# Performance work log

Measured on AMD Instinct MI355X. Metric: run time of the kernel, lower is better.

The kernel has to match this reference:

```python
import jax, jax.numpy as jnp
import numpy as np
from jax import lax

THR = 1.0
BETA = 0.9
SLOPE = 25.0  # fast_sigmoid surrogate slope
N_JOINTS = 6

@jax.custom_vjp
def spike_fn(x):
    # Heaviside forward, fast_sigmoid surrogate backward (snntorch surrogate.fast_sigmoid)
    return (x > 0).astype(x.dtype)

def _spike_fwd(x):
    return spike_fn(x), x

def _spike_bwd(x, g):
    return (g / (SLOPE * jnp.abs(x) + 1.0) ** 2,)

spike_fn.defvjp(_spike_fwd, _spike_bwd)

def lif(cur, mem):
    # snntorch Leaky, reset_mechanism='subtract': reset from previous mem (detached)
    reset = lax.stop_gradient(spike_fn(mem - THR))
    mem = BETA * mem + cur - reset * THR
    spk = spike_fn(mem - THR)
    return spk, mem

def rate_encode(data, u):
    # data: (B, F), u: (T, B, F) uniform[0,1) -> binary spikes (T, B, F)
    dmin = jnp.min(data, axis=1, keepdims=True)
    dmax = jnp.max(data, axis=1, keepdims=True)
    rng = dmax - dmin
    rng = jnp.where(rng == 0, jnp.ones_like(rng), rng)
    norm = (data - dmin) / rng
    prob = jnp.clip(100.0 * norm * 0.001, 0.0, 1.0)  # max_rate=100, dt=0.001
    return (u < prob[None]).astype(jnp.float32)

def conv1x1(x, W, b):
    # x: (B, Cin, H, 1), W: (Cout, Cin, 1, 1)
    y = lax.conv_general_dilated(x, W, (1, 1), 'VALID',
                                 dimension_numbers=('NCHW', 'OIHW', 'NCHW'))
    return y + b[None, :, None, None]

def setup_inputs() -> dict:
    key = jax.random.key(0)
    ks = jax.random.split(key, 16)
    B, T, n = 8192, 200, N_JOINTS
    inp = {
        'x':  jax.random.normal(ks[0], (B, 3 * n), jnp.float32),
        'u1': jax.random.uniform(ks[1], (T, B, 2 * n), jnp.float32),
        'u2': jax.random.uniform(ks[2], (T, B, n), jnp.float32),
        'u3': jax.random.uniform(ks[3], (T, B, n), jnp.float32),
        'W1': jax.random.normal(ks[4], (256, 12), jnp.float32) * 0.2,
        'b1': jax.random.normal(ks[5], (256,), jnp.float32) * 0.05,
        'W2': jax.random.normal(ks[6], (256, 256), jnp.float32) * 0.06,
        'b2': jax.random.normal(ks[7], (256,), jnp.float32) * 0.05,
        'W3': jax.random.normal(ks[8], (6, 256), jnp.float32) * 0.06,
        'b3': jax.random.normal(ks[9], (6,), jnp.float32) * 0.05,
        'Wc1': jax.random.normal(ks[10], (32, 3, 1, 1), jnp.float32) * 0.5,
        'bc1': jax.random.normal(ks[11], (32,), jnp.float32) * 0.05,
        'Wc2': jax.random.normal(ks[12], (64, 32, 1, 1), jnp.float32) * 0.15,
        'bc2': jax.random.normal(ks[13], (64,), jnp.float32) * 0.05,
        'WA': jax.random.normal(ks[14], (1, 64), jnp.float32) * 0.12,
    }
    return inp

def reference(x, u1, u2, u3, W1, b1, W2, b2, W3, b3, Wc1, bc1, Wc2, bc2, WA):
    n = N_JOINTS
    B = x.shape[0]
    spk_in = rate_encode(x[:, :2 * n], u1)        # (T, B, 2n)
    spk_thdot = rate_encode(x[:, n:2 * n], u2)    # (T, B, n)
    spk_thdot2 = rate_encode(x[:, 2 * n:], u3)    # (T, B, n)

    mem1 = jnp.zeros((B, 256), jnp.float32)
    mem2 = jnp.zeros((B, 256), jnp.float32)
    mem3 = jnp.zeros((B, n), jnp.float32)
    mem4 = jnp.zeros((B, 32, n, 1), jnp.float32)
    conv_out0 = jnp.zeros((B, 64, n, 1), jnp.float32)

    def step(carry, inp):
        m1, m2, m3, m4, _ = carry
        s_in, s_td, s_td2 = inp
        spk1, m1 = lif(s_in @ W1.T + b1, m1)
        spk2, m2 = lif(spk1 @ W2.T + b2, m2)
        spk3, m3 = lif(spk2 @ W3.T + b3, m3)
        spk_conv = jnp.stack([s_td, spk3, s_td2], axis=1)[..., None]  # (B,3,n,1)
        cur4 = conv1x1(spk_conv, Wc1, bc1)  # maxpool1 with k=1 is identity
        spk4, m4 = lif(cur4, m4)
        conv_out = conv1x1(spk4, Wc2, bc2)  # maxpool2 with k=1 is identity
        return (m1, m2, m3, m4, conv_out), None

    (_, _, _, _, conv_out), _ = lax.scan(step, (mem1, mem2, mem3, mem4, conv_out0),
                                         (spk_in, spk_thdot, spk_thdot2))
    # c.T: out_a/b/c = fc_A(conv_out[:, :, i, 0]) for i in 0..2, no bias
    c_t = jnp.einsum('bcm,c->bm', conv_out[:, :, :3, 0], WA[0])  # (B, 3)
    return c_t
```

## Files before the change

### kernel.cpp

```cpp
#include <hip/hip_runtime.h>
#include <cstdint>
#include <cstddef>

typedef unsigned long long u64;

__global__ void prep_weights(const float* __restrict__ W2, const float* __restrict__ Wc2,
                             const float* __restrict__ bc2, const float* __restrict__ WA,
                             float* __restrict__ Wt2f, double* __restrict__ wEff,
                             double* __restrict__ bEff)
{
  int id = blockIdx.x * 256 + (int)threadIdx.x;
  if (id < 65536){ int i = id >> 8, j = id & 255; Wt2f[(i<<8)+j] = W2[j*256+i]; }
  else if (id < 65792){ Wt2f[id] = 0.0f; }
  if (id < 32){ double s = 0.0; for (int c=0;c<64;c++) s += (double)WA[c]*(double)Wc2[c*32+id]; wEff[id] = s; }
  if (id == 32){ double s = 0.0; for (int c=0;c<64;c++) s += (double)WA[c]*(double)bc2[c]; *bEff = s; }
}

__global__ void prep_probs(const float* __restrict__ x, double* __restrict__ probs, int B)
{
  int b = blockIdx.x, k = (int)threadIdx.x;
  if (b >= B || k >= 24) return;
  double* pb = probs + (size_t)b*24;
  if (k >= 18){ pb[k] = -1.0; return; }
  int fk, g0, gn;
  if (k < 12){ fk = k;          g0 = 0;  gn = 12; }
  else if (k < 15){ fk = 6+(k-12);  g0 = 6;  gn = 6; }
  else           { fk = 12+(k-15); g0 = 12; gn = 6; }
  const float* xb = x + (size_t)b*18;
  double mn = (double)xb[g0], mx = mn;
  for (int f = 1; f < gn; f++){ double v = (double)xb[g0+f]; mn = fmin(mn, v); mx = fmax(mx, v); }
  double rng = mx - mn; if (rng == 0.0) rng = 1.0;
  double norm = ((double)xb[fk] - mn) / rng;
  double p = (100.0 * norm) * 0.001;
  p = fmin(fmax(p, 0.0), 1.0);
  pb[k] = p;
}

__global__ void prep_enc(const float* __restrict__ u1, const float* __restrict__ u2,
                         const float* __restrict__ u3, const double* __restrict__ probs,
                         unsigned* __restrict__ encT, int B, int T)
{
  int b = blockIdx.x * blockDim.x + (int)threadIdx.x;
  int t = blockIdx.y;
  if (b >= B) return;
  if (t >= T){ encT[(size_t)b*(T+2) + t] = 0u; return; }
  const double* pb = probs + (size_t)b*24;
  size_t r = (size_t)t * B + b;
  const float* a1 = u1 + r*12;
  const float* a2 = u2 + r*6;
  const float* a3 = u3 + r*6;
  unsigned e = 0;
  #pragma unroll
  for (int k = 0; k < 12; k++) if ((double)a1[k] < pb[k])    e |= (1u << k);
  #pragma unroll
  for (int h = 0; h < 3; h++)  if ((double)a2[h] < pb[12+h]) e |= (1u << (12+h));
  #pragma unroll
  for (int h = 0; h < 3; h++)  if ((double)a3[h] < pb[15+h]) e |= (1u << (15+h));
  encT[(size_t)b*(T+2) + t] = e;
}

__global__ __launch_bounds__(256) void snn_main(
    const unsigned* __restrict__ encT,
    const float* __restrict__ b1, const float* __restrict__ b2, const float* __restrict__ b3,
    const float* __restrict__ W1, const float* __restrict__ W3,
    const float* __restrict__ Wc1, const float* __restrict__ bc1,
    const float* __restrict__ Wt2f,
    const double* __restrict__ wEff, const double* __restrict__ bEff,
    float* __restrict__ out, int B, int T)
{
  __shared__ __align__(16) float s_w1[12*256];
  __shared__ __align__(16) float s_w3[257*4];

  const int tid  = (int)threadIdx.x;
  const int lane = tid & 63;
  const int wid  = tid >> 6;
  const int b = blockIdx.x * 4 + wid;
  const int l4 = lane << 2;
  const int lcl = (lane < 3) ? lane : 3;

  for (int i = tid; i < 3072; i += 256){ int k = i >> 8, j = i & 255; s_w1[i] = W1[j*12+k]; }
  for (int i = tid; i < 1028; i += 256){
    int r = i >> 2, c = i & 3;
    s_w3[i] = (r < 256 && c < 3) ? W3[c*256 + r] : 0.0f;
  }
  __syncthreads();
  if (b >= B) return;

  const float4 b1f = *(const float4*)(b1 + l4);
  const float4 b2f = *(const float4*)(b2 + l4);
  const double b1d0=b1f.x, b1d1=b1f.y, b1d2=b1f.z, b1d3=b1f.w;
  const double b2d0=b2f.x, b2d1=b2f.y, b2d2=b2f.z, b2d3=b2f.w;
  const double b3d = (lane < 3) ? (double)b3[lane] : 0.0;
  double wc1b=0.0, wEd=0.0, pre0=0.0, pre1=0.0, pre2=0.0, pre3=0.0;
  if (lane < 32){
    double wa = (double)Wc1[lane*3+0];
    wc1b      = (double)Wc1[lane*3+1];
    double wc = (double)Wc1[lane*3+2];
    double bd = (double)bc1[lane];
    wEd  = wEff[lane];
    pre0 = bd;
    pre1 = bd + wa;
    pre2 = bd + wc;
    pre3 = bd + wa + wc;
  }

  double m10=0,m11=0,m12=0,m13=0;
  double m20=0,m21=0,m22=0,m23=0;
  double m3v=0;
  double m40=0,m41=0,m42=0;
  bool sp20=false,sp21=false,sp22=false,sp23=false;
  bool sp3v=false;
  bool sp40=false,sp41=false,sp42=false;

  const unsigned* encTb = encT + (size_t)b * (T + 2);

  unsigned e_cur = __builtin_amdgcn_readfirstlane(encTb[0]);
  unsigned e_nx  = __builtin_amdgcn_readfirstlane(encTb[1]);
  double ca0=b1d0, ca1=b1d1, ca2=b1d2, ca3=b1d3;
  {
    unsigned w = e_cur & 0xFFFu;
    while (w){
      int k = __builtin_ctz(w); w &= w-1;
      const float4 r = *(const float4*)&s_w1[(k<<8) + l4];
      ca0 += (double)r.x; ca1 += (double)r.y; ca2 += (double)r.z; ca3 += (double)r.w;
    }
  }

  for (int t = 0; t < T; t++){
    m10 = fma(0.9, m10, ca0);
    m11 = fma(0.9, m11, ca1);
    m12 = fma(0.9, m12, ca2);
    m13 = fma(0.9, m13, ca3);
    const bool sp10 = m10 > 1.0; u64 w0 = __ballot(sp10);
    const bool sp11 = m11 > 1.0; u64 w1 = __ballot(sp11);
    const bool sp12 = m12 > 1.0; u64 w2 = __ballot(sp12);
    const bool sp13 = m13 > 1.0; u64 w3m = __ballot(sp13);

    int i0 = w0  ? (((int)__builtin_ctzll(w0) <<2)|0) : 256;  w0  &= w0 -1;
    int i1 = w1  ? (((int)__builtin_ctzll(w1) <<2)|1) : 256;  w1  &= w1 -1;
    int i2 = w2  ? (((int)__builtin_ctzll(w2) <<2)|2) : 256;  w2  &= w2 -1;
    int i3 = w3m ? (((int)__builtin_ctzll(w3m)<<2)|3) : 256;  w3m &= w3m-1;
    const float4 g0 = *(const float4*)(Wt2f + ((size_t)i0<<8) + l4);
    const float4 g1 = *(const float4*)(Wt2f + ((size_t)i1<<8) + l4);
    const float4 g2 = *(const float4*)(Wt2f + ((size_t)i2<<8) + l4);
    const float4 g3 = *(const float4*)(Wt2f + ((size_t)i3<<8) + l4);

    const unsigned e_n2 = encTb[t+2];

    ca0 = (sp10 ? -1.0 : 0.0) + b1d0;
    ca1 = (sp11 ? -1.0 : 0.0) + b1d1;
    ca2 = (sp12 ? -1.0 : 0.0) + b1d2;
    ca3 = (sp13 ? -1.0 : 0.0) + b1d3;
    {
      unsigned w = e_nx & 0xFFFu;
      while (w){
        int k = __builtin_ctz(w); w &= w-1;
        const float4 r = *(const float4*)&s_w1[(k<<8) + l4];
        ca0 += (double)r.x; ca1 += (double)r.y; ca2 += (double)r.z; ca3 += (double)r.w;
      }
    }

    double c0 = (sp20 ? -1.0 : 0.0) + b2d0;
    double c1 = (sp21 ? -1.0 : 0.0) + b2d1;
    double c2 = (sp22 ? -1.0 : 0.0) + b2d2;
    double c3 = (sp23 ? -1.0 : 0.0) + b2d3;
    if (i0 != 256){ c0 += (double)g0.x; c1 += (double)g0.y; c2 += (double)g0.z; c3 += (double)g0.w; }
    if (i1 != 256){ c0 += (double)g1.x; c1 += (double)g1.y; c2 += (double)g1.z; c3 += (double)g1.w; }
    if (i2 != 256){ c0 += (double)g2.x; c1 += (double)g2.y; c2 += (double)g2.z; c3 += (double)g2.w; }
    if (i3 != 256){ c0 += (double)g3.x; c1 += (double)g3.y; c2 += (double)g3.z; c3 += (double)g3.w; }

    while (w0 | w1 | w2 | w3m){
      int j0 = w0  ? (((int)__builtin_ctzll(w0) <<2)|0) : 256;  w0  &= w0 -1;
      int j1 = w1  ? (((int)__builtin_ctzll(w1) <<2)|1) : 256;  w1  &= w1 -1;
      int j2 = w2  ? (((int)__builtin_ctzll(w2) <<2)|2) : 256;  w2  &= w2 -1;
      int j3 = w3m ? (((int)__builtin_ctzll(w3m)<<2)|3) : 256;  w3m &= w3m-1;
      const float4 h0 = *(const float4*)(Wt2f + ((size_t)j0<<8) + l4);
      const float4 h1 = *(const float4*)(Wt2f + ((size_t)j1<<8) + l4);
      const float4 h2 = *(const float4*)(Wt2f + ((size_t)j2<<8) + l4);
      const float4 h3 = *(const float4*)(Wt2f + ((size_t)j3<<8) + l4);
      if (j0 != 256){ c0 += (double)h0.x; c1 += (double)h0.y; c2 += (double)h0.z; c3 += (double)h0.w; }
      if (j1 != 256){ c0 += (double)h1.x; c1 += (double)h1.y; c2 += (double)h1.z; c3 += (double)h1.w; }
      if (j2 != 256){ c0 += (double)h2.x; c1 += (double)h2.y; c2 += (double)h2.z; c3 += (double)h2.w; }
      if (j3 != 256){ c0 += (double)h3.x; c1 += (double)h3.y; c2 += (double)h3.z; c3 += (double)h3.w; }
    }

    m20 = fma(0.9, m20, c0);
    m21 = fma(0.9, m21, c1);
    m22 = fma(0.9, m22, c2);
    m23 = fma(0.9, m23, c3);
    sp20 = m20 > 1.0; u64 v0 = __ballot(sp20);
    sp21 = m21 > 1.0; u64 v1 = __ballot(sp21);
    sp22 = m22 > 1.0; u64 v2 = __ballot(sp22);
    sp23 = m23 > 1.0; u64 v3 = __ballot(sp23);

    double cl3 = (sp3v ? -1.0 : 0.0) + b3d;
    while (v0 | v1 | v2 | v3){
      int j0 = v0 ? (((int)__builtin_ctzll(v0)<<2)|0) : 256;  v0 &= v0-1;
      int j1 = v1 ? (((int)__builtin_ctzll(v1)<<2)|1) : 256;  v1 &= v1-1;
      int j2 = v2 ? (((int)__builtin_ctzll(v2)<<2)|2) : 256;  v2 &= v2-1;
      int j3 = v3 ? (((int)__builtin_ctzll(v3)<<2)|3) : 256;  v3 &= v3-1;
      if (j0 != 256) cl3 += (double)s_w3[(j0<<2) + lcl];
      if (j1 != 256) cl3 += (double)s_w3[(j1<<2) + lcl];
      if (j2 != 256) cl3 += (double)s_w3[(j2<<2) + lcl];
      if (j3 != 256) cl3 += (double)s_w3[(j3<<2) + lcl];
    }
    m3v = fma(0.9, m3v, cl3);
    sp3v = m3v > 1.0;
    const unsigned s3 = (unsigned)(__ballot((lane < 3) && sp3v) & 7ull);

    const unsigned td  = (e_cur >> 12) & 7u;
    const unsigned td2 = (e_cur >> 15) & 7u;
    {
      double cur, t1, t2;
      t1 = (td2 & 1u) ? pre2 : pre0;  t2 = (td2 & 1u) ? pre3 : pre1;
      cur = (td & 1u) ? t2 : t1;
      if (s3 & 1u) cur += wc1b;
      cur += sp40 ? -1.0 : 0.0;
      m40 = fma(0.9, m40, cur); sp40 = m40 > 1.0;
      t1 = (td2 & 2u) ? pre2 : pre0;  t2 = (td2 & 2u) ? pre3 : pre1;
      cur = (td & 2u) ? t2 : t1;
      if (s3 & 2u) cur += wc1b;
      cur += sp41 ? -1.0 : 0.0;
      m41 = fma(0.9, m41, cur); sp41 = m41 > 1.0;
      t1 = (td2 & 4u) ? pre2 : pre0;  t2 = (td2 & 4u) ? pre3 : pre1;
      cur = (td & 4u) ? t2 : t1;
      if (s3 & 4u) cur += wc1b;
      cur += sp42 ? -1.0 : 0.0;
      m42 = fma(0.9, m42, cur); sp42 = m42 > 1.0;
    }

    e_cur = e_nx;
    e_nx  = __builtin_amdgcn_readfirstlane(e_n2);
  }

  double o0 = sp40 ? wEd : 0.0;
  double o1 = sp41 ? wEd : 0.0;
  double o2 = sp42 ? wEd : 0.0;
  for (int off = 32; off > 0; off >>= 1){
    o0 += __shfl_xor(o0, off, 64);
    o1 += __shfl_xor(o1, off, 64);
    o2 += __shfl_xor(o2, off, 64);
  }
  if (lane == 0){
    const double be = *bEff;
    out[b*3+0] = (float)(o0 + be);
    out[b*3+1] = (float)(o1 + be);
    out[b*3+2] = (float)(o2 + be);
  }
}

extern "C" void kernel_launch(void* const* d_in, const int* in_sizes, int n_in,
                              void* d_out, int out_size, void* d_ws, size_t ws_size,
                              hipStream_t stream)
{
  const float* x   = (const float*)d_in[0];
  const float* u1  = (const float*)d_in[1];
  const float* u2  = (const float*)d_in[2];
  const float* u3  = (const float*)d_in[3];
  const float* W1  = (const float*)d_in[4];
  const float* b1  = (const float*)d_in[5];
  const float* W2  = (const float*)d_in[6];
  const float* b2  = (const float*)d_in[7];
  const float* W3  = (const float*)d_in[8];
  const float* b3  = (const float*)d_in[9];
  const float* Wc1 = (const float*)d_in[10];
  const float* bc1 = (const float*)d_in[11];
  const float* Wc2 = (const float*)d_in[12];
  const float* bc2 = (const float*)d_in[13];
  const float* WA  = (const float*)d_in[14];
  float* out = (float*)d_out;

  const int B = in_sizes[0] / 18;
  const int T = in_sizes[1] / (B * 12);

  char* ws = (char*)d_ws;
  float*  Wt2f  = (float*)(ws + 0);
  double* wEff  = (double*)(ws + 263168);
  double* bEff  = (double*)(ws + 263424);
  double* probs = (double*)(ws + 263432);
  unsigned* encT= (unsigned*)(ws + 263432 + (size_t)B*24*8);

  hipLaunchKernelGGL(prep_weights, dim3(257), dim3(256), 0, stream,
                     W2, Wc2, bc2, WA, Wt2f, wEff, bEff);
  hipLaunchKernelGGL(prep_probs, dim3(B), dim3(64), 0, stream, x, probs, B);
  hipLaunchKernelGGL(prep_enc, dim3((B+255)/256, T+2), dim3(256), 0, stream,
                     u1, u2, u3, probs, encT, B, T);
  hipLaunchKernelGGL(snn_main, dim3((B+3)/4), dim3(256), 0, stream,
                     encT, b1, b2, b3, W1, W3, Wc1, bc1, Wt2f, wEff, bEff, out, B, T);
}
```

Before: 684.1 us.

## Replace layer-1 sparse W1 accumulation with precomputed 6-bit subset-sum table lookups

Precomputes a table of double-precision partial sums of W1 columns for every 6-bit spike pattern (two halves of the 12 input bits), then replaces the per-step data-dependent loop over input spikes in shared memory with two table-row gathers from global memory, prefetched one step ahead. This removes the variable-length LDS loop and its per-bit conversions from the serial time loop. In exchange it adds a small prep kernel, 256 KB of workspace, and global/L2 loads of doubles each step. The summation order changes, which can alter rounding slightly.

Result: slower. 710.3 us (+3.8%).

```diff
diff --git a/kernel.cpp b/kernel.cpp
--- a/kernel.cpp
+++ b/kernel.cpp
@@ -14,6 +14,18 @@
   else if (id < 65792){ Wt2f[id] = 0.0f; }
   if (id < 32){ double s = 0.0; for (int c=0;c<64;c++) s += (double)WA[c]*(double)Wc2[c*32+id]; wEff[id] = s; }
   if (id == 32){ double s = 0.0; for (int c=0;c<64;c++) s += (double)WA[c]*(double)bc2[c]; *bEff = s; }
+}
+
+__global__ void prep_tab(const float* __restrict__ W1, double* __restrict__ Stab)
+{
+  int id = blockIdx.x * 256 + (int)threadIdx.x;
+  if (id >= 32768) return;
+  int h = id >> 14, m = (id >> 8) & 63, j = id & 255;
+  double s = 0.0;
+  #pragma unroll
+  for (int k = 0; k < 6; k++)
+    if ((m >> k) & 1) s += (double)W1[j*12 + 6*h + k];
+  Stab[id] = s;
 }
 
 __global__ void prep_probs(const float* __restrict__ x, double* __restrict__ probs, int B)
@@ -62,13 +74,12 @@
 __global__ __launch_bounds__(256) void snn_main(
     const unsigned* __restrict__ encT,
     const float* __restrict__ b1, const float* __restrict__ b2, const float* __restrict__ b3,
-    const float* __restrict__ W1, const float* __restrict__ W3,
+    const float* __restrict__ W3,
     const float* __restrict__ Wc1, const float* __restrict__ bc1,
-    const float* __restrict__ Wt2f,
+    const float* __restrict__ Wt2f, const double* __restrict__ Stab,
     const double* __restrict__ wEff, const double* __restrict__ bEff,
     float* __restrict__ out, int B, int T)
 {
-  __shared__ __align__(16) float s_w1[12*256];
   __shared__ __align__(16) float s_w3[257*4];
 
   const int tid  = (int)threadIdx.x;
@@ -78,7 +89,6 @@
   const int l4 = lane << 2;
   const int lcl = (lane < 3) ? lane : 3;
 
-  for (int i = tid; i < 3072; i += 256){ int k = i >> 8, j = i & 255; s_w1[i] = W1[j*12+k]; }
   for (int i = tid; i < 1028; i += 256){
     int r = i >> 2, c = i & 3;
     s_w3[i] = (r < 256 && c < 3) ? W3[c*256 + r] : 0.0f;
@@ -88,8 +98,6 @@
 
   const float4 b1f = *(const float4*)(b1 + l4);
   const float4 b2f = *(const float4*)(b2 + l4);
-  const double b1d0=b1f.x, b1d1=b1f.y, b1d2=b1f.z, b1d3=b1f.w;
-  const double b2d0=b2f.x, b2d1=b2f.y, b2d2=b2f.z, b2d3=b2f.w;
   const double b3d = (lane < 3) ? (double)b3[lane] : 0.0;
   double wc1b=0.0, wEd=0.0, pre0=0.0, pre1=0.0, pre2=0.0, pre3=0.0;
   if (lane < 32){
@@ -108,6 +116,7 @@
   double m20=0,m21=0,m22=0,m23=0;
   double m3v=0;
   double m40=0,m41=0,m42=0;
+  bool sp10=false,sp11=false,sp12=false,sp13=false;
   bool sp20=false,sp21=false,sp22=false,sp23=false;
   bool sp3v=false;
   bool sp40=false,sp41=false,sp42=false;
@@ -116,25 +125,21 @@
 
   unsigned e_cur = __builtin_amdgcn_readfirstlane(encTb[0]);
   unsigned e_nx  = __builtin_amdgcn_readfirstlane(encTb[1]);
-  double ca0=b1d0, ca1=b1d1, ca2=b1d2, ca3=b1d3;
-  {
-    unsigned w = e_cur & 0xFFFu;
-    while (w){
-      int k = __builtin_ctz(w); w &= w-1;
-      const float4 r = *(const float4*)&s_w1[(k<<8) + l4];
-      ca0 += (double)r.x; ca1 += (double)r.y; ca2 += (double)r.z; ca3 += (double)r.w;
-    }
-  }
+
+  const double* rowL0 = Stab + ((size_t)(e_cur & 63u) << 8);
+  const double* rowH0 = Stab + ((size_t)(64u + ((e_cur >> 6) & 63u)) << 8);
+  double2 loA = *(const double2*)(rowL0 + l4), loB = *(const double2*)(rowL0 + l4 + 2);
+  double2 hiA = *(const double2*)(rowH0 + l4), hiB = *(const double2*)(rowH0 + l4 + 2);
 
   for (int t = 0; t < T; t++){
-    m10 = fma(0.9, m10, ca0);
-    m11 = fma(0.9, m11, ca1);
-    m12 = fma(0.9, m12, ca2);
-    m13 = fma(0.9, m13, ca3);
-    const bool sp10 = m10 > 1.0; u64 w0 = __ballot(sp10);
-    const bool sp11 = m11 > 1.0; u64 w1 = __ballot(sp11);
-    const bool sp12 = m12 > 1.0; u64 w2 = __ballot(sp12);
-    const bool sp13 = m13 > 1.0; u64 w3m = __ballot(sp13);
+    m10 = fma(0.9, m10, (sp10 ? -1.0 : 0.0) + (double)b1f.x + loA.x + hiA.x);
+    m11 = fma(0.9, m11, (sp11 ? -1.0 : 0.0) + (double)b1f.y + loA.y + hiA.y);
+    m12 = fma(0.9, m12, (sp12 ? -1.0 : 0.0) + (double)b1f.z + loB.x + hiB.x);
+    m13 = fma(0.9, m13, (sp13 ? -1.0 : 0.0) + (double)b1f.w + loB.y + hiB.y);
+    sp10 = m10 > 1.0; u64 w0  = __ballot(sp10);
+    sp11 = m11 > 1.0; u64 w1  = __ballot(sp11);
+    sp12 = m12 > 1.0; u64 w2  = __ballot(sp12);
+    sp13 = m13 > 1.0; u64 w3m = __ballot(sp13);
 
     int i0 = w0  ? (((int)__builtin_ctzll(w0) <<2)|0) : 256;  w0  &= w0 -1;
     int i1 = w1  ? (((int)__builtin_ctzll(w1) <<2)|1) : 256;  w1  &= w1 -1;
@@ -145,25 +150,17 @@
     const float4 g2 = *(const float4*)(Wt2f + ((size_t)i2<<8) + l4);
     const float4 g3 = *(const float4*)(Wt2f + ((size_t)i3<<8) + l4);
 
+    const double* rowLn = Stab + ((size_t)(e_nx & 63u) << 8);
+    const double* rowHn = Stab + ((size_t)(64u + ((e_nx >> 6) & 63u)) << 8);
+    const double2 loAn = *(const double2*)(rowLn + l4), loBn = *(const double2*)(rowLn + l4 + 2);
+    const double2 hiAn = *(const double2*)(rowHn + l4), hiBn = *(const double2*)(rowHn + l4 + 2);
+
     const unsigned e_n2 = encTb[t+2];
 
-    ca0 = (sp10 ? -1.0 : 0.0) + b1d0;
-    ca1 = (sp11 ? -1.0 : 0.0) + b1d1;
-    ca2 = (sp12 ? -1.0 : 0.0) + b1d2;
-    ca3 = (sp13 ? -1.0 : 0.0) + b1d3;
-    {
-      unsigned w = e_nx & 0xFFFu;
-      while (w){
-        int k = __builtin_ctz(w); w &= w-1;
-        const float4 r = *(const float4*)&s_w1[(k<<8) + l4];
-        ca0 += (double)r.x; ca1 += (double)r.y; ca2 += (double)r.z; ca3 += (double)r.w;
-      }
-    }
-
-    double c0 = (sp20 ? -1.0 : 0.0) + b2d0;
-    double c1 = (sp21 ? -1.0 : 0.0) + b2d1;
-    double c2 = (sp22 ? -1.0 : 0.0) + b2d2;
-    double c3 = (sp23 ? -1.0 : 0.0) + b2d3;
+    double c0 = (sp20 ? -1.0 : 0.0) + (double)b2f.x;
+    double c1 = (sp21 ? -1.0 : 0.0) + (double)b2f.y;
+    double c2 = (sp22 ? -1.0 : 0.0) + (double)b2f.z;
+    double c3 = (sp23 ? -1.0 : 0.0) + (double)b2f.w;
     if (i0 != 256){ c0 += (double)g0.x; c1 += (double)g0.y; c2 += (double)g0.z; c3 += (double)g0.w; }
     if (i1 != 256){ c0 += (double)g1.x; c1 += (double)g1.y; c2 += (double)g1.z; c3 += (double)g1.w; }
     if (i2 != 256){ c0 += (double)g2.x; c1 += (double)g2.y; c2 += (double)g2.z; c3 += (double)g2.w; }
@@ -229,6 +226,7 @@
       m42 = fma(0.9, m42, cur); sp42 = m42 > 1.0;
     }
 
+    loA = loAn; loB = loBn; hiA = hiAn; hiB = hiBn;
     e_cur = e_nx;
     e_nx  = __builtin_amdgcn_readfirstlane(e_n2);
   }
@@ -275,16 +273,18 @@
 
   char* ws = (char*)d_ws;
   float*  Wt2f  = (float*)(ws + 0);
-  double* wEff  = (double*)(ws + 263168);
-  double* bEff  = (double*)(ws + 263424);
-  double* probs = (double*)(ws + 263432);
-  unsigned* encT= (unsigned*)(ws + 263432 + (size_t)B*24*8);
+  double* Stab  = (double*)(ws + 263168);
+  double* wEff  = (double*)(ws + 525312);
+  double* bEff  = (double*)(ws + 525568);
+  double* probs = (double*)(ws + 525576);
+  unsigned* encT= (unsigned*)(ws + 525576 + (size_t)B*24*8);
 
   hipLaunchKernelGGL(prep_weights, dim3(257), dim3(256), 0, stream,
                      W2, Wc2, bc2, WA, Wt2f, wEff, bEff);
+  hipLaunchKernelGGL(prep_tab, dim3(128), dim3(256), 0, stream, W1, Stab);
   hipLaunchKernelGGL(prep_probs, dim3(B), dim3(64), 0, stream, x, probs, B);
   hipLaunchKernelGGL(prep_enc, dim3((B+255)/256, T+2), dim3(256), 0, stream,
                      u1, u2, u3, probs, encT, B, T);
   hipLaunchKernelGGL(snn_main, dim3((B+3)/4), dim3(256), 0, stream,
-                     encT, b1, b2, b3, W1, W3, Wc1, bc1, Wt2f, wEff, bEff, out, B, T);
-}
+                     encT, b1, b2, b3, W3, Wc1, bc1, Wt2f, Stab, wEff, bEff, out, B, T);
+}
```
